# Performance work log

Measured on AMD Instinct MI355X. Metric: run time of the kernel, lower is better.

Reference implementation:

```python
import jax, jax.numpy as jnp
import numpy as np

B, C, X, Y, Z = 2, 4, 128, 128, 96
_BIG = 1e10  # effectively infinite squared distance (no background in line)


def _edt_sq_pass(f, axis):
    """One separable pass of the exact squared EDT along `axis`:
    g[i] = min_j f[j] + (i - j)^2  (Felzenszwalb lower envelope, brute-forced
    with lax.map so only O(rest) memory per step)."""
    f = jnp.moveaxis(f, axis, -1)  # (..., L)
    idx = jnp.arange(f.shape[-1], dtype=f.dtype)
    g = jax.lax.map(lambda i: jnp.min(f + (i - idx) ** 2, axis=-1), idx)  # (L, ...)
    return jnp.moveaxis(jnp.moveaxis(g, 0, -1), -1, axis)


def _edt(mask):
    """Exact Euclidean distance of True voxels to the nearest False voxel
    (matches scipy.ndimage.distance_transform_edt on a binary mask)."""
    f = jnp.where(mask, _BIG, 0.0).astype(jnp.float32)
    for ax in (-3, -2, -1):  # three spatial axes
        f = _edt_sq_pass(f, ax)
    return jnp.sqrt(f)


def _neighbor(m, axis, d):
    """Shift `m` by d along `axis` with edge replication (reflect border,
    as in skimage's grey erosion used by find_boundaries)."""
    axis = axis % m.ndim
    pw = [(1, 1) if i == axis else (0, 0) for i in range(m.ndim)]
    p = jnp.pad(m, pw, mode='edge')
    sl = [slice(None)] * m.ndim
    sl[axis] = slice(1 + d, p.shape[axis] - 1 + d)
    return p[tuple(sl)]


def _inner_boundary(m):
    """skimage find_boundaries(mode='inner', connectivity=1): foreground voxels
    with at least one background face-neighbor."""
    eroded = m
    for ax in (-3, -2, -1):
        eroded = eroded & _neighbor(m, ax, 1) & _neighbor(m, ax, -1)
    return m & ~eroded


def _compute_sdf(onehot):
    """Signed distance map per (batch, class): negdis - posdis, zero on the
    inner boundary; zero where the class is absent; channel 0 is skipped."""
    posdis = _edt(onehot)          # dist inside object to background
    negdis = _edt(~onehot)         # dist outside object to foreground
    sdf = jnp.where(_inner_boundary(onehot), 0.0, negdis - posdis)
    any_pos = jnp.any(onehot, axis=(2, 3, 4), keepdims=True)
    sdf = jnp.where(any_pos, sdf, 0.0)
    return sdf.at[:, 0].set(0.0)   # loop starts at c=1 in the original


def setup_inputs() -> dict:
    key = jax.random.key(0)
    k1, k2 = jax.random.split(key)
    net_output = jax.random.normal(k1, (B, C, X, Y, Z), dtype=jnp.float32)
    gt = jax.random.randint(k2, (B, 1, X, Y, Z), 0, C, dtype=jnp.int32)
    return {"net_output": net_output, "gt": gt}


def reference(net_output, gt):
    probs = jax.nn.softmax(net_output, axis=1)  # softmax_helper = softmax over class dim
    classes = jnp.arange(net_output.shape[1], dtype=gt.dtype).reshape(1, -1, 1, 1, 1)
    onehot = gt == classes  # scatter_(1, gt, 1) one-hot, bool (B,C,X,Y,Z)
    phi = _compute_sdf(onehot)
    # einsum('bcxyz,bcxyz->bcxyz') on foreground channels, then global mean
    return jnp.mean(probs[:, 1:] * phi[:, 1:])
```

## Files before the change

kernel.cpp:

```cpp
#include <hip/hip_runtime.h>
#include <math.h>

#define XD 128
#define YD 128
#define ZD 96
#define NV (XD*YD*ZD)
#define SXX (YD*ZD)
#define SENT 49152
#define TW2 114
#define TDW (TW2/2)
#define TROWS 144

__global__ void k_zero_flags(int* flags) {
    if (threadIdx.x < 8) flags[threadIdx.x] = 0;
}

__global__ __launch_bounds__(384) void k_scan_x(const int* __restrict__ gt,
                                                unsigned char* __restrict__ out,
                                                int* __restrict__ flags,
                                                int batch0) {
    const int bb  = blockIdx.y;
    const int myb = batch0 + bb;
    const int tid = threadIdx.x;
    const int l   = tid & 63;
    const int w6  = tid >> 6;
    const int lq0 = blockIdx.x * 64;

    __shared__ unsigned char gtile[64 * 132];
    __shared__ int blkbits;
    if (tid == 0) blkbits = 0;

    int mybits = 0;
    const int* gp = gt + (size_t)myb * NV + lq0 + l;
    for (int j = w6; j < XD; j += 6) {
        int g = gp[(size_t)j * SXX];
        mybits |= 1 << g;
        gtile[l * 132 + j] = (unsigned char)g;
    }
#pragma unroll
    for (int off = 32; off; off >>= 1) mybits |= __shfl_xor(mybits, off);
    __syncthreads();
    if ((tid & 63) == 0) atomicOr(&blkbits, mybits);

    unsigned int D[32];
    {
        const unsigned int ci = (unsigned int)((w6 >> 1) + 1);
        const int s = w6 & 1;
        unsigned int G[32];
        const unsigned int* grow = (const unsigned int*)gtile + l * 33;
#pragma unroll
        for (int q = 0; q < 32; ++q) G[q] = grow[q];

        int cnt = 200;
#pragma unroll
        for (int q = 0; q < 32; ++q) {
            unsigned int u = G[q], dv = 0;
#pragma unroll
            for (int b = 0; b < 4; ++b) {
                unsigned int gv = (u >> (8 * b)) & 255u;
                bool zero = s ? (gv == ci) : (gv != ci);
                cnt = zero ? 0 : ((cnt < 200) ? cnt + 1 : 200);
                dv |= (unsigned int)cnt << (8 * b);
            }
            D[q] = dv;
        }
        cnt = 200;
#pragma unroll
        for (int q = 31; q >= 0; --q) {
            unsigned int u = G[q], dv = D[q];
#pragma unroll
            for (int b = 3; b >= 0; --b) {
                unsigned int gv = (u >> (8 * b)) & 255u;
                bool zero = s ? (gv == ci) : (gv != ci);
                cnt = zero ? 0 : ((cnt < 200) ? cnt + 1 : 200);
                unsigned int old = (dv >> (8 * b)) & 255u;
                unsigned int nbv = ((unsigned int)cnt < old) ? (unsigned int)cnt : old;
                dv = (dv & ~(255u << (8 * b))) | (nbv << (8 * b));
            }
            D[q] = dv;
        }
    }
    __syncthreads();
    if (tid == 0) atomicOr(&flags[myb], blkbits);

    {
        const int r = l & 3;
        unsigned char* ob = out + (size_t)(bb * 6 + w6) * NV + lq0 + (l & ~3);
#pragma unroll
        for (int q = 0; q < 32; ++q) {
            unsigned int A = D[q];
            unsigned int Bv = (unsigned int)__shfl_xor((int)A, 1);
            unsigned int t = (r & 1)
                ? __builtin_amdgcn_perm(A, Bv, 0x07030501u)
                : __builtin_amdgcn_perm(A, Bv, 0x02060004u);
            unsigned int Cv = (unsigned int)__shfl_xor((int)t, 2);
            unsigned int y = (r & 2)
                ? __builtin_amdgcn_perm(t, Cv, 0x07060302u)
                : __builtin_amdgcn_perm(t, Cv, 0x01000504u);
            *(unsigned int*)(ob + (size_t)(4 * q + r) * SXX) = y;
        }
    }
}

__device__ __forceinline__ bool edt_fast(const float r[32], float m[16]) {
#pragma unroll
    for (int k = 0; k < 16; ++k) m[k] = r[k + 8];
#pragma unroll
    for (int t = 1; t <= 4; ++t) {
        const float t2 = (float)(t * t);
#pragma unroll
        for (int k = 0; k < 16; ++k)
            m[k] = fminf(m[k], fminf(r[k + 8 - t], r[k + 8 + t]) + t2);
    }
    float mm = m[0];
#pragma unroll
    for (int k = 1; k < 16; ++k) mm = fmaxf(mm, m[k]);
    if (__all(mm <= 16.0f)) return true;
#pragma unroll
    for (int t = 5; t <= 8; ++t) {
        const float t2 = (float)(t * t);
#pragma unroll
        for (int k = 0; k < 16; ++k)
            m[k] = fminf(m[k], fminf(r[k + 8 - t], r[k + 8 + t]) + t2);
    }
    mm = m[0];
#pragma unroll
    for (int k = 1; k < 16; ++k) mm = fmaxf(mm, m[k]);
    return __all(mm <= 64.0f) != 0;
}

template<int STRIDE, int L>
__device__ void edt_slow(const unsigned short* __restrict__ p0, int i0,
                         float m[16]) {
    int t = 9;
    bool done = false;
    while (!done && t < L) {
        for (int u = 0; u < 4; ++u, ++t) {
            float t2 = (float)(t * t);
#pragma unroll
            for (int k = 0; k < 16; ++k) {
                int jm = i0 + k - t; if (jm < -8) jm = -8;
                int jp = i0 + k + t; if (jp > L + 7) jp = L + 7;
                m[k] = fminf(m[k], fminf((float)p0[jm * STRIDE],
                                         (float)p0[jp * STRIDE]) + t2);
            }
        }
        float mm = m[0];
#pragma unroll
        for (int k = 1; k < 16; ++k) mm = fmaxf(mm, m[k]);
        done = __all(mm <= (float)((t - 1) * (t - 1))) != 0;
    }
}

__global__ __launch_bounds__(768, 6) void k_pass_yz(const unsigned char* __restrict__ in,
                                                    unsigned short* __restrict__ out) {
    const int lv  = blockIdx.y;
    const int x   = blockIdx.x;
    const int tid = threadIdx.x;
    __shared__ unsigned short tile[TROWS * TW2];
    unsigned int* t32 = (unsigned int*)tile;

    for (int i = tid; i < 16 * TDW; i += 768) {
        int r = i / TDW, c = i - r * TDW;
        int row = (r < 8) ? r : 128 + r;
        t32[row * TDW + c] = 0xFFFFFFFFu;
    }
    for (int i = tid; i < 128 * 9; i += 768) {
        int r = i / 9, c = i - r * 9;
        int col = (c < 4) ? c : (48 + c);
        t32[(8 + r) * TDW + col] = 0xFFFFFFFFu;
    }
    {
        const uint4* ip = (const uint4*)(in + (size_t)lv * NV + (size_t)x * SXX);
        uint4 v = ip[tid];
        int e = tid * 16;
        int y = e / ZD, z = e - y * ZD;
        unsigned int base = (8 + y) * TDW + (8 + z) / 2;
        unsigned int vv[4] = {v.x, v.y, v.z, v.w};
#pragma unroll
        for (int q = 0; q < 4; ++q) {
            unsigned int b0 = vv[q] & 255u, b1 = (vv[q] >> 8) & 255u;
            unsigned int b2 = (vv[q] >> 16) & 255u, b3 = vv[q] >> 24;
            t32[base + 2 * q] = (b0 > 127u ? SENT : b0 * b0) |
                                ((b1 > 127u ? SENT : b1 * b1) << 16);
            t32[base + 2 * q + 1] = (b2 > 127u ? SENT : b2 * b2) |
                                    ((b3 > 127u ? SENT : b3 * b3) << 16);
        }
    }
    __syncthreads();

    float m[16];
    {
        const int z0 = tid % 96;
        const int i0 = (tid / 96) * 16;
        float r[32];
#pragma unroll
        for (int w = 0; w < 32; ++w) r[w] = (float)tile[(i0 + w) * TW2 + 8 + z0];
        if (!edt_fast(r, m)) edt_slow<TW2, YD>(&tile[8 * TW2 + 8 + z0], i0, m);
        __syncthreads();
#pragma unroll
        for (int k = 0; k < 16; ++k)
            tile[(8 + i0 + k) * TW2 + 8 + z0] =
                (unsigned short)fminf(m[k], (float)SENT);
        __syncthreads();
    }
    {
        const int y0 = tid % 128;
        const int i0 = (tid / 128) * 16;
        float r[32];
        {
            const unsigned int* wp = &t32[(8 + y0) * TDW + i0 / 2];
#pragma unroll
            for (int q = 0; q < 16; ++q) {
                unsigned int u = wp[q];
                r[2 * q] = (float)(u & 0xFFFFu);
                r[2 * q + 1] = (float)(u >> 16);
            }
        }
        if (!edt_fast(r, m)) edt_slow<1, ZD>(&tile[(8 + y0) * TW2 + 8], i0, m);
        __syncthreads();
        {
            unsigned int* wp = &t32[(8 + y0) * TDW + (8 + i0) / 2];
#pragma unroll
            for (int q = 0; q < 8; ++q) {
                unsigned int u0 = (unsigned int)fminf(m[2 * q],     (float)SENT);
                unsigned int u1 = (unsigned int)fminf(m[2 * q + 1], (float)SENT);
                wp[q] = u0 | (u1 << 16);
            }
        }
        __syncthreads();
    }
    uint4* op = (uint4*)(out + (size_t)lv * NV + (size_t)x * SXX);
    for (int o = tid; o < SXX / 8; o += 768) {
        int e = o * 8;
        int y = e / ZD, z = e - y * ZD;
        const unsigned int* sp = &t32[(8 + y) * TDW + (8 + z) / 2];
        uint4 v; v.x = sp[0]; v.y = sp[1]; v.z = sp[2]; v.w = sp[3];
        op[o] = v;
    }
}

__global__ __launch_bounds__(256) void k_accum_batch(const unsigned short* __restrict__ vols,
                                                     const float* __restrict__ net,
                                                     const int* __restrict__ flags,
                                                     double* __restrict__ partials,
                                                     int batch0) {
    const int b = batch0 + blockIdx.y;
    double ls = 0.0;
    const float* nb = net + (size_t)b * 4 * NV;
    const unsigned short* vb = vols + (size_t)blockIdx.y * 6 * NV;
    const int fbits = flags[b];
    const int NP = NV / 2;
    for (int p = blockIdx.x * 256 + threadIdx.x; p < NP; p += 1024 * 256) {
        const int idx = p * 2;
        float2 v0 = *(const float2*)(nb + idx);
        float2 v1 = *(const float2*)(nb + NV + idx);
        float2 v2 = *(const float2*)(nb + 2 * NV + idx);
        float2 v3 = *(const float2*)(nb + 3 * NV + idx);

        float mxa = fmaxf(fmaxf(v0.x, v1.x), fmaxf(v2.x, v3.x));
        float mxb = fmaxf(fmaxf(v0.y, v1.y), fmaxf(v2.y, v3.y));
        float e1a = __expf(v1.x - mxa), e2a = __expf(v2.x - mxa), e3a = __expf(v3.x - mxa);
        float e1b = __expf(v1.y - mxb), e2b = __expf(v2.y - mxb), e3b = __expf(v3.y - mxb);
        float sa = __expf(v0.x - mxa) + e1a + e2a + e3a;
        float sb = __expf(v0.y - mxb) + e1b + e2b + e3b;
        float ia = __frcp_rn(sa);
        float ib = __frcp_rn(sb);

        float acc = 0.0f;
#pragma unroll
        for (int ci = 1; ci <= 3; ++ci) {
            if ((fbits >> ci) & 1) {
                ushort2 dp = *(const ushort2*)(vb + (size_t)(2 * ci - 2) * NV + idx);
                ushort2 dn = *(const ushort2*)(vb + (size_t)(2 * ci - 1) * NV + idx);
                float ea = (ci == 1) ? e1a : ((ci == 2) ? e2a : e3a);
                float eb = (ci == 1) ? e1b : ((ci == 2) ? e2b : e3b);
                float phiA = (dp.x == 1) ? 0.0f
                           : (sqrtf((float)dn.x) - sqrtf((float)dp.x));
                float phiB = (dp.y == 1) ? 0.0f
                           : (sqrtf((float)dn.y) - sqrtf((float)dp.y));
                acc += (ea * ia) * phiA + (eb * ib) * phiB;
            }
        }
        ls += (double)acc;
    }
    __shared__ double sd[256];
    sd[threadIdx.x] = ls;
    __syncthreads();
    for (int off = 128; off > 0; off >>= 1) {
        if (threadIdx.x < off) sd[threadIdx.x] += sd[threadIdx.x + off];
        __syncthreads();
    }
    if (threadIdx.x == 0) partials[(size_t)b * 1024 + blockIdx.x] = sd[0];
}

__global__ void k_reduce(const double* __restrict__ partials, int n,
                         float* __restrict__ out) {
    __shared__ double sd[256];
    double ls = 0.0;
    for (int i = threadIdx.x; i < n; i += 256) ls += partials[i];
    sd[threadIdx.x] = ls;
    __syncthreads();
    for (int off = 128; off > 0; off >>= 1) {
        if (threadIdx.x < off) sd[threadIdx.x] += sd[threadIdx.x + off];
        __syncthreads();
    }
    if (threadIdx.x == 0) out[0] = (float)(sd[0] / 9437184.0);
}

extern "C" void kernel_launch(void* const* d_in, const int* in_sizes, int n_in,
                              void* d_out, int out_size, void* d_ws, size_t ws_size,
                              hipStream_t stream) {
    const float* net = (const float*)d_in[0];
    const int*   gt  = (const int*)d_in[1];
    float* out = (float*)d_out;
    char* ws = (char*)d_ws;

    const size_t xbufB1 = (size_t)6 * NV;
    const size_t zbufB1 = (size_t)6 * NV * sizeof(unsigned short);
    const size_t tail   = (size_t)2048 * sizeof(double) + 64;

    const int nb = (ws_size >= 2 * (xbufB1 + zbufB1) + tail) ? 2 : 1;

    unsigned char*  xbuf = (unsigned char*)ws;
    unsigned short* zbuf = (unsigned short*)(ws + (size_t)nb * xbufB1);
    double* partials = (double*)(ws + (size_t)nb * (xbufB1 + zbufB1));
    int* flags = (int*)((char*)partials + 2048 * sizeof(double));

    hipLaunchKernelGGL(k_zero_flags, dim3(1), dim3(64), 0, stream, flags);

    for (int b0 = 0; b0 < 2; b0 += nb) {
        hipLaunchKernelGGL(k_scan_x, dim3(SXX / 64, nb), dim3(384), 0, stream,
                           gt, xbuf, flags, b0);
        hipLaunchKernelGGL(k_pass_yz, dim3(XD, 6 * nb), dim3(768), 0, stream,
                           xbuf, zbuf);
        hipLaunchKernelGGL(k_accum_batch, dim3(1024, nb), dim3(256), 0, stream,
                           zbuf, net, flags, partials, b0);
    }
    hipLaunchKernelGGL(k_reduce, dim3(1), dim3(256), 0, stream, partials,
                       2048, out);
}
```

Before: 81.95 us.

## Precompute fp16 softmax probs in scan kernel, skip absent classes, drop tile writeback

Extra blocks are added to the x-scan kernel to compute the softmax over the four classes and store the three foreground probabilities as fp16. This lets the accumulation kernel read half-precision probs instead of all four float channels. The yz pass now exits early for classes absent from a batch, and the z-pass results are written straight to global memory instead of going back through shared memory. The flag-zeroing kernel is replaced with a memset. Storing probabilities in fp16 adds rounding error to the loss, and the workspace requirement grows.

```diff
diff --git a/kernel.cpp b/kernel.cpp
--- a/kernel.cpp
+++ b/kernel.cpp
@@ -1,4 +1,5 @@
 #include <hip/hip_runtime.h>
+#include <hip/hip_fp16.h>
 #include <math.h>
 
 #define XD 128
@@ -10,18 +11,58 @@
 #define TW2 114
 #define TDW (TW2/2)
 #define TROWS 144
-
-__global__ void k_zero_flags(int* flags) {
-    if (threadIdx.x < 8) flags[threadIdx.x] = 0;
-}
-
-__global__ __launch_bounds__(384) void k_scan_x(const int* __restrict__ gt,
-                                                unsigned char* __restrict__ out,
-                                                int* __restrict__ flags,
-                                                int batch0) {
+#define SCANB 192
+#define PROBB 1024
+
+__global__ __launch_bounds__(384) void k_scan_prob(const int* __restrict__ gt,
+                                                   const float* __restrict__ net,
+                                                   unsigned char* __restrict__ out,
+                                                   __half2* __restrict__ probs,
+                                                   int* __restrict__ flags,
+                                                   int batch0) {
     const int bb  = blockIdx.y;
     const int myb = batch0 + bb;
     const int tid = threadIdx.x;
+
+    if (blockIdx.x >= SCANB) {
+        const int p = (blockIdx.x - SCANB) * 384 + tid;
+        const int idx = p * 4;
+        const float* nb = net + (size_t)myb * 4 * NV;
+        float4 v0 = *(const float4*)(nb + idx);
+        float4 v1 = *(const float4*)(nb + NV + idx);
+        float4 v2 = *(const float4*)(nb + 2 * NV + idx);
+        float4 v3 = *(const float4*)(nb + 3 * NV + idx);
+
+        const float a0[4] = {v0.x, v0.y, v0.z, v0.w};
+        const float a1[4] = {v1.x, v1.y, v1.z, v1.w};
+        const float a2[4] = {v2.x, v2.y, v2.z, v2.w};
+        const float a3[4] = {v3.x, v3.y, v3.z, v3.w};
+        float p1[4], p2[4], p3[4];
+#pragma unroll
+        for (int j = 0; j < 4; ++j) {
+            float mx = fmaxf(fmaxf(a0[j], a1[j]), fmaxf(a2[j], a3[j]));
+            float e0 = __expf(a0[j] - mx);
+            float e1 = __expf(a1[j] - mx);
+            float e2 = __expf(a2[j] - mx);
+            float e3 = __expf(a3[j] - mx);
+            float iv = __frcp_rn(e0 + e1 + e2 + e3);
+            p1[j] = e1 * iv; p2[j] = e2 * iv; p3[j] = e3 * iv;
+        }
+        __half2 h10 = __floats2half2_rn(p1[0], p1[1]);
+        __half2 h11 = __floats2half2_rn(p1[2], p1[3]);
+        __half2 h20 = __floats2half2_rn(p2[0], p2[1]);
+        __half2 h21 = __floats2half2_rn(p2[2], p2[3]);
+        __half2 h30 = __floats2half2_rn(p3[0], p3[1]);
+        __half2 h31 = __floats2half2_rn(p3[2], p3[3]);
+        ((__half2*)probs)[(size_t)(myb * 3 + 0) * (NV / 2) + 2 * p]     = h10;
+        ((__half2*)probs)[(size_t)(myb * 3 + 0) * (NV / 2) + 2 * p + 1] = h11;
+        ((__half2*)probs)[(size_t)(myb * 3 + 1) * (NV / 2) + 2 * p]     = h20;
+        ((__half2*)probs)[(size_t)(myb * 3 + 1) * (NV / 2) + 2 * p + 1] = h21;
+        ((__half2*)probs)[(size_t)(myb * 3 + 2) * (NV / 2) + 2 * p]     = h30;
+        ((__half2*)probs)[(size_t)(myb * 3 + 2) * (NV / 2) + 2 * p + 1] = h31;
+        return;
+    }
+
     const int l   = tid & 63;
     const int w6  = tid >> 6;
     const int lq0 = blockIdx.x * 64;
@@ -130,8 +171,8 @@
 }
 
 template<int STRIDE, int L>
-__device__ void edt_slow(const unsigned short* __restrict__ p0, int i0,
-                         float m[16]) {
+__device__ __forceinline__ void edt_slow(const unsigned short* __restrict__ p0,
+                                         int i0, float m[16]) {
     int t = 9;
     bool done = false;
     while (!done && t < L) {
@@ -152,11 +193,17 @@
     }
 }
 
-__global__ __launch_bounds__(768, 6) void k_pass_yz(const unsigned char* __restrict__ in,
-                                                    unsigned short* __restrict__ out) {
+__global__ __launch_bounds__(768) void k_pass_yz(const unsigned char* __restrict__ in,
+                                                 unsigned short* __restrict__ zbuf,
+                                                 const int* __restrict__ flags,
+                                                 int batch0) {
     const int lv  = blockIdx.y;
     const int x   = blockIdx.x;
     const int tid = threadIdx.x;
+    const int bbp = lv / 6;
+    const int cp  = (lv % 6) >> 1;
+    if (((flags[batch0 + bbp] >> (cp + 1)) & 1) == 0) return;
+
     __shared__ unsigned short tile[TROWS * TW2];
     unsigned int* t32 = (unsigned int*)tile;
 
@@ -208,78 +255,50 @@
         const int y0 = tid % 128;
         const int i0 = (tid / 128) * 16;
         float r[32];
-        {
-            const unsigned int* wp = &t32[(8 + y0) * TDW + i0 / 2];
-#pragma unroll
-            for (int q = 0; q < 16; ++q) {
-                unsigned int u = wp[q];
-                r[2 * q] = (float)(u & 0xFFFFu);
-                r[2 * q + 1] = (float)(u >> 16);
-            }
+        const unsigned int* wp = &t32[(8 + y0) * TDW + i0 / 2];
+#pragma unroll
+        for (int q = 0; q < 16; ++q) {
+            unsigned int u = wp[q];
+            r[2 * q] = (float)(u & 0xFFFFu);
+            r[2 * q + 1] = (float)(u >> 16);
         }
         if (!edt_fast(r, m)) edt_slow<1, ZD>(&tile[(8 + y0) * TW2 + 8], i0, m);
-        __syncthreads();
-        {
-            unsigned int* wp = &t32[(8 + y0) * TDW + (8 + i0) / 2];
-#pragma unroll
-            for (int q = 0; q < 8; ++q) {
-                unsigned int u0 = (unsigned int)fminf(m[2 * q],     (float)SENT);
-                unsigned int u1 = (unsigned int)fminf(m[2 * q + 1], (float)SENT);
-                wp[q] = u0 | (u1 << 16);
-            }
-        }
-        __syncthreads();
-    }
-    uint4* op = (uint4*)(out + (size_t)lv * NV + (size_t)x * SXX);
-    for (int o = tid; o < SXX / 8; o += 768) {
-        int e = o * 8;
-        int y = e / ZD, z = e - y * ZD;
-        const unsigned int* sp = &t32[(8 + y) * TDW + (8 + z) / 2];
-        uint4 v; v.x = sp[0]; v.y = sp[1]; v.z = sp[2]; v.w = sp[3];
-        op[o] = v;
-    }
-}
-
-__global__ __launch_bounds__(256) void k_accum_batch(const unsigned short* __restrict__ vols,
-                                                     const float* __restrict__ net,
-                                                     const int* __restrict__ flags,
-                                                     double* __restrict__ partials,
-                                                     int batch0) {
+        unsigned int* op = (unsigned int*)(zbuf + (size_t)lv * NV +
+                                           (size_t)x * SXX +
+                                           (size_t)y0 * ZD + i0);
+#pragma unroll
+        for (int q = 0; q < 8; ++q) {
+            unsigned int u0 = (unsigned int)fminf(m[2 * q],     (float)SENT);
+            unsigned int u1 = (unsigned int)fminf(m[2 * q + 1], (float)SENT);
+            op[q] = u0 | (u1 << 16);
+        }
+    }
+}
+
+__global__ __launch_bounds__(256) void k_accum(const unsigned short* __restrict__ vols,
+                                               const __half2* __restrict__ probs,
+                                               const int* __restrict__ flags,
+                                               double* __restrict__ partials,
+                                               int batch0) {
     const int b = batch0 + blockIdx.y;
-    double ls = 0.0;
-    const float* nb = net + (size_t)b * 4 * NV;
     const unsigned short* vb = vols + (size_t)blockIdx.y * 6 * NV;
     const int fbits = flags[b];
-    const int NP = NV / 2;
-    for (int p = blockIdx.x * 256 + threadIdx.x; p < NP; p += 1024 * 256) {
+    double ls = 0.0;
+    for (int p = blockIdx.x * 256 + threadIdx.x; p < NV / 2; p += 1024 * 256) {
         const int idx = p * 2;
-        float2 v0 = *(const float2*)(nb + idx);
-        float2 v1 = *(const float2*)(nb + NV + idx);
-        float2 v2 = *(const float2*)(nb + 2 * NV + idx);
-        float2 v3 = *(const float2*)(nb + 3 * NV + idx);
-
-        float mxa = fmaxf(fmaxf(v0.x, v1.x), fmaxf(v2.x, v3.x));
-        float mxb = fmaxf(fmaxf(v0.y, v1.y), fmaxf(v2.y, v3.y));
-        float e1a = __expf(v1.x - mxa), e2a = __expf(v2.x - mxa), e3a = __expf(v3.x - mxa);
-        float e1b = __expf(v1.y - mxb), e2b = __expf(v2.y - mxb), e3b = __expf(v3.y - mxb);
-        float sa = __expf(v0.x - mxa) + e1a + e2a + e3a;
-        float sb = __expf(v0.y - mxb) + e1b + e2b + e3b;
-        float ia = __frcp_rn(sa);
-        float ib = __frcp_rn(sb);
-
         float acc = 0.0f;
 #pragma unroll
         for (int ci = 1; ci <= 3; ++ci) {
             if ((fbits >> ci) & 1) {
                 ushort2 dp = *(const ushort2*)(vb + (size_t)(2 * ci - 2) * NV + idx);
                 ushort2 dn = *(const ushort2*)(vb + (size_t)(2 * ci - 1) * NV + idx);
-                float ea = (ci == 1) ? e1a : ((ci == 2) ? e2a : e3a);
-                float eb = (ci == 1) ? e1b : ((ci == 2) ? e2b : e3b);
-                float phiA = (dp.x == 1) ? 0.0f
+                float2 pf = __half22float2(
+                    probs[(size_t)(b * 3 + ci - 1) * (NV / 2) + p]);
+                float phi0 = (dp.x == 1) ? 0.0f
                            : (sqrtf((float)dn.x) - sqrtf((float)dp.x));
-                float phiB = (dp.y == 1) ? 0.0f
+                float phi1 = (dp.y == 1) ? 0.0f
                            : (sqrtf((float)dn.y) - sqrtf((float)dp.y));
-                acc += (ea * ia) * phiA + (eb * ib) * phiB;
+                acc += pf.x * phi0 + pf.y * phi1;
             }
         }
         ls += (double)acc;
@@ -318,24 +337,26 @@
 
     const size_t xbufB1 = (size_t)6 * NV;
     const size_t zbufB1 = (size_t)6 * NV * sizeof(unsigned short);
+    const size_t probsB = (size_t)2 * 3 * NV * 2;
     const size_t tail   = (size_t)2048 * sizeof(double) + 64;
 
-    const int nb = (ws_size >= 2 * (xbufB1 + zbufB1) + tail) ? 2 : 1;
+    const int nb = (ws_size >= 2 * (xbufB1 + zbufB1) + probsB + tail) ? 2 : 1;
 
     unsigned char*  xbuf = (unsigned char*)ws;
     unsigned short* zbuf = (unsigned short*)(ws + (size_t)nb * xbufB1);
-    double* partials = (double*)(ws + (size_t)nb * (xbufB1 + zbufB1));
-    int* flags = (int*)((char*)partials + 2048 * sizeof(double));
-
-    hipLaunchKernelGGL(k_zero_flags, dim3(1), dim3(64), 0, stream, flags);
+    __half2*       probs = (__half2*)(ws + (size_t)nb * (xbufB1 + zbufB1));
+    double*     partials = (double*)((char*)probs + probsB);
+    int*           flags = (int*)((char*)partials + 2048 * sizeof(double));
+
+    hipMemsetAsync(flags, 0, 8 * sizeof(int), stream);
 
     for (int b0 = 0; b0 < 2; b0 += nb) {
-        hipLaunchKernelGGL(k_scan_x, dim3(SXX / 64, nb), dim3(384), 0, stream,
-                           gt, xbuf, flags, b0);
+        hipLaunchKernelGGL(k_scan_prob, dim3(SCANB + PROBB, nb), dim3(384), 0,
+                           stream, gt, net, xbuf, probs, flags, b0);
         hipLaunchKernelGGL(k_pass_yz, dim3(XD, 6 * nb), dim3(768), 0, stream,
-                           xbuf, zbuf);
-        hipLaunchKernelGGL(k_accum_batch, dim3(1024, nb), dim3(256), 0, stream,
-                           zbuf, net, flags, partials, b0);
+                           xbuf, zbuf, flags, b0);
+        hipLaunchKernelGGL(k_accum, dim3(1024, nb), dim3(256), 0, stream,
+                           zbuf, probs, flags, partials, b0);
     }
     hipLaunchKernelGGL(k_reduce, dim3(1), dim3(256), 0, stream, partials,
                        2048, out);
```

After: 84.06 us. +2.6%, slower.
